# Optimization experiments

Hardware: AMD Instinct MI355X
Metric: run time of the kernel (lower is better)

The kernel has to match this reference:

```python
import jax, jax.numpy as jnp
import numpy as np

CP_SPACING = (4, 4, 4)
SIGMAS = tuple(0.44 * cp for cp in CP_SPACING)


def _gaussian_kernel_3d(sigmas):
    # Faithful to DeepReg layer_util.gaussian_filter_3d
    ks = [int(np.ceil(s * 3) + np.mod(np.ceil(s * 3) + 1, 2)) for s in sigmas]
    grid = np.stack(np.meshgrid(*[np.arange(k) for k in ks], indexing="ij"), axis=0)  # [3,k,k,k]
    mean = ((np.asarray(ks, np.float64) - 1.0) / 2.0).reshape(-1, 1, 1, 1)
    var = (np.asarray(sigmas, np.float64) ** 2.0).reshape(-1, 1, 1, 1)
    norm = 1.0 / (np.sqrt(2.0 * np.pi) ** 3 + np.prod(sigmas))  # as in DeepReg source
    kernel = norm * np.exp(-np.sum((grid - mean) ** 2.0 / (2.0 * var), axis=0))
    kernel = kernel / np.sum(kernel)  # sums to 1
    return kernel.astype(np.float32)  # [k,k,k]


def setup_inputs() -> dict:
    key = jax.random.key(0)
    image = jax.random.normal(key, (4, 160, 160, 160, 3), dtype=jnp.float32)  # DDF volume, 3 channels
    kernel = jnp.asarray(_gaussian_kernel_3d(SIGMAS))  # deterministic [7,7,7] Gaussian buffer
    return {"image": image, "kernel": kernel}


def reference(image, kernel):
    b, d1, d2, d3, c = image.shape
    # DeepReg's [k,k,k,3,3] diagonal kernel == depthwise blur per channel.
    kdw = jnp.tile(kernel[..., None, None], (1, 1, 1, 1, c))  # [k,k,k,1,C]
    blurred = jax.lax.conv_general_dilated(
        image, kdw,
        window_strides=(1, 1, 1),
        padding="SAME",
        dimension_numbers=("NDHWC", "DHWIO", "NDHWC"),
        feature_group_count=c,
    )
    # output control-point grid: ceil(dim / cp_spacing) + 3
    size = tuple(int(np.ceil(v / cp)) + 3 for v, cp in zip((d1, d2, d3), CP_SPACING))
    # tf.image.resize bilinear (TF2) uses half-pixel centers == jax.image.resize 'linear'
    out = jax.image.resize(blurred, (b,) + size + (c,), method="linear")
    return out
```

## Files before the change

kernel.cpp:

```cpp
#include <hip/hip_runtime.h>
#include <hip/hip_fp16.h>

#define NB 4
#define NI 160
#define NO 43
#define NC 3
#define KS 7
#define KPAD 3
#define MT 16
#define CH 8
#define CH1 2
#define P1B 64
#define NP 22

#define ROWF (NI * NC)
#define PROW 132
#define PROW4 (PROW / 4)
#define LROW 484
#define SLICE (NO * NO * NC)

#define A1H_BYTES ((size_t)NB * NI * NI * PROW * 2)
#define A2H_BYTES ((size_t)NB * NI * NO * PROW * 2)
#define P2P_THREADS ((size_t)NB * NI * NP * PROW4)
#define P3_THREADS ((size_t)NB * NO * NO * PROW4)

struct __align__(16) Tables {
    float w1[NO][MT];
    float wp[NP][24][2];
    int   o1hp[NP][24];
    int   o0h[NO][MT];
    int   j3[NO];
    int   jlo[NO];
};

constexpr double ctaylor(double r) {
    double s = 1.0, term = 1.0;
    for (int n = 1; n <= 13; ++n) { term *= r / (double)n; s += term; }
    return s;
}
constexpr double cexp_neg(double x) {
    double y = -x;
    int k = (int)(y * 16.0);
    double r = y - (double)k / 16.0;
    double e16 = ctaylor(1.0 / 16.0);
    double p = 1.0;
    for (int i = 0; i < k; ++i) p *= e16;
    return 1.0 / (p * ctaylor(r));
}
constexpr int cceil(double x)  { int c = (int)x; return ((double)c < x) ? c + 1 : c; }
constexpr int cfloor(double x) { int f = (int)x; return ((double)f > x) ? f - 1 : f; }
constexpr double cabsd(double x) { return x < 0 ? -x : x; }

constexpr double comp_w(int j, double sf, int ilo, int ihi, const double* g) {
    if (j >= NI || j < 0) return 0.0;
    double cw = 0.0;
    for (int t = 0; t < KS; ++t) {
        int i = j + KPAD - t;
        if (i >= ilo && i <= ihi) {
            double w = 1.0 - cabsd(sf - (double)i) * (43.0 / 160.0);
            if (w > 0.0) cw += g[t] * w;
        }
    }
    return cw;
}

struct Band { double sf; int ilo; int ihi; double wsum; };
constexpr Band bandof(int o) {
    const double inv_scale = 160.0 / 43.0;
    double sf = ((double)o + 0.5) * inv_scale - 0.5;
    int ilo = cceil(sf - inv_scale);  if (ilo < 0) ilo = 0;
    int ihi = cfloor(sf + inv_scale); if (ihi > NI - 1) ihi = NI - 1;
    double wsum = 0.0;
    for (int i = ilo; i <= ihi; ++i) {
        double w = 1.0 - cabsd(sf - (double)i) * (43.0 / 160.0);
        if (w > 0.0) wsum += w;
    }
    return {sf, ilo, ihi, wsum};
}

constexpr Tables make_tables() {
    Tables T{};
    double g[KS] = {};
    double gs = 0.0;
    const double sig = 0.44 * 4.0;
    for (int i = 0; i < KS; ++i) {
        double d = (double)i - 3.0;
        g[i] = cexp_neg(-(d * d) / (2.0 * sig * sig));
        gs += g[i];
    }
    for (int i = 0; i < KS; ++i) g[i] /= gs;

    for (int o = 0; o < NO; ++o) {
        Band B = bandof(o);
        int jlo = B.ilo - KPAD; if (jlo < 0) jlo = 0;
        T.j3[o] = jlo & ~3;
        T.jlo[o] = jlo;
        for (int k = 0; k < MT; ++k) {
            int j = jlo + k;
            T.w1[o][k] = (float)(comp_w(j, B.sf, B.ilo, B.ihi, g) / B.wsum);
            int jc = (j < NI) ? j : (NI - 1);
            T.o0h[o][k] = jc * (NO * PROW * 2);
        }
    }
    for (int p = 0; p < NP; ++p) {
        int oA = 2 * p, oB = 2 * p + 1;
        Band BA = bandof(oA);
        int jp = T.j3[oA];
        for (int k = 0; k < 24; ++k) {
            T.wp[p][k][0] = (float)(comp_w(jp + k, BA.sf, BA.ilo, BA.ihi, g) / BA.wsum);
            if (oB < NO) {
                Band BB = bandof(oB);
                T.wp[p][k][1] = (float)(comp_w(jp + k, BB.sf, BB.ilo, BB.ihi, g) / BB.wsum);
            } else {
                T.wp[p][k][1] = 0.0f;
            }
            int jc = (jp + k < NI) ? (jp + k) : (NI - 1);
            T.o1hp[p][k] = jc * (PROW * 2);
        }
    }
    return T;
}

__constant__ Tables dT = make_tables();

struct __align__(8) h4 { __half2 lo, hi; };
union h2u { __half2 h; unsigned int u; };

__global__ __launch_bounds__(P1B) void k_p1(
        const float* __restrict__ img, __half* __restrict__ A1h) {
    __shared__ __align__(16) float rows[CH1 * LROW + 64];
    int t = threadIdx.x;
    int blk = blockIdx.x;

    const int p = t % NP, row = t / NP;
    const bool has = (t < NP * CH1);

    float4 wq0, wq1, wq2, wq3, wq4, wq5, wq6, wq7, wq8, wq9, wq10, wq11;
    int jp = 0;
    if (has) {
        jp = dT.j3[2 * p];
        const float4* wpp = (const float4*)dT.wp[p];
        wq0 = wpp[0];  wq1 = wpp[1];  wq2 = wpp[2];  wq3 = wpp[3];
        wq4 = wpp[4];  wq5 = wpp[5];  wq6 = wpp[6];  wq7 = wpp[7];
        wq8 = wpp[8];  wq9 = wpp[9];  wq10 = wpp[10]; wq11 = wpp[11];
    }

    const float4* src = (const float4*)(img + (size_t)blk * (CH1 * ROWF));
    for (int g = t; g < CH1 * ROWF / 4; g += P1B) {
        int r = g / 120, m = g % 120;
        *(float4*)(rows + r * LROW + 4 * m) = src[g];
    }
    if (t < CH1 * 4) rows[(t >> 2) * LROW + ROWF + (t & 3)] = 0.f;
    rows[CH1 * LROW + t] = 0.f;
    __syncthreads();

    if (has) {
        const float4* dp = (const float4*)(rows + row * LROW + 3 * jp);
        float a0 = 0.f, a1 = 0.f, a2 = 0.f;
        float b0 = 0.f, b1 = 0.f, b2 = 0.f;
#define STEP(M, WQA, WQB) {                                                    \
            float4 v0 = dp[3*(M)], v1 = dp[3*(M)+1], v2 = dp[3*(M)+2];         \
            a0 += WQA.x * v0.x; a1 += WQA.x * v0.y; a2 += WQA.x * v0.z;        \
            b0 += WQA.y * v0.x; b1 += WQA.y * v0.y; b2 += WQA.y * v0.z;        \
            a0 += WQA.z * v0.w; a1 += WQA.z * v1.x; a2 += WQA.z * v1.y;        \
            b0 += WQA.w * v0.w; b1 += WQA.w * v1.x; b2 += WQA.w * v1.y;        \
            a0 += WQB.x * v1.z; a1 += WQB.x * v1.w; a2 += WQB.x * v2.x;        \
            b0 += WQB.y * v1.z; b1 += WQB.y * v1.w; b2 += WQB.y * v2.x;        \
            a0 += WQB.z * v2.y; a1 += WQB.z * v2.z; a2 += WQB.z * v2.w;        \
            b0 += WQB.w * v2.y; b1 += WQB.w * v2.z; b2 += WQB.w * v2.w;        \
        }
        STEP(0, wq0, wq1)  STEP(1, wq2, wq3)  STEP(2, wq4, wq5)
        STEP(3, wq6, wq7)  STEP(4, wq8, wq9)  STEP(5, wq10, wq11)
#undef STEP
        h2u c0, c1, c2;
        c0.h = __floats2half2_rn(a0, a1);
        c1.h = __floats2half2_rn(a2, b0);
        c2.h = __floats2half2_rn(b1, b2);
        unsigned int* dstu = (unsigned int*)A1h;
        size_t baseu = ((size_t)blk * CH1 + row) * (PROW / 2) + 3 * p;
        dstu[baseu] = c0.u; dstu[baseu + 1] = c1.u; dstu[baseu + 2] = c2.u;
    }
}

__device__ __forceinline__ int xcd_swz(int wg, int nwg) {
    int q = nwg >> 3, r = nwg & 7;
    int x = wg & 7, i = wg >> 3;
    return (x < r ? x * (q + 1) : r * (q + 1) + (x - r) * q) + i;
}

__global__ __launch_bounds__(256) void k_p2(
        const __half* __restrict__ A1h, __half* __restrict__ A2h) {
    int blk = xcd_swz(blockIdx.x, gridDim.x);
    size_t idx = (size_t)blk * 256 + threadIdx.x;
    if (idx >= P2P_THREADS) return;
    int ii = (int)idx;
    int col4 = ii % PROW4;
    int p    = (ii / PROW4) % NP;
    int slab = ii / (PROW4 * NP);
    const char* base = (const char*)A1h + ((size_t)slab * NI * PROW + col4 * 4) * 2;
    const float4* wpp = (const float4*)dT.wp[p];
    const int4*   ot  = (const int4*)dT.o1hp[p];
    float4 wq0 = wpp[0], wq1 = wpp[1], wq2 = wpp[2],  wq3 = wpp[3];
    float4 wq4 = wpp[4], wq5 = wpp[5], wq6 = wpp[6],  wq7 = wpp[7];
    float4 wq8 = wpp[8], wq9 = wpp[9], wq10 = wpp[10], wq11 = wpp[11];
    int4 t0 = ot[0], t1 = ot[1], t2 = ot[2], t3 = ot[3], t4 = ot[4], t5 = ot[5];
    float4 a = {0.f,0.f,0.f,0.f}, b = a;
#define TP(J, WA, WB) { h4 v = *(const h4*)(base + (unsigned)(J));             \
        float2 f0 = __half22float2(v.lo), f1 = __half22float2(v.hi);           \
        a.x += (WA) * f0.x; a.y += (WA) * f0.y;                                \
        a.z += (WA) * f1.x; a.w += (WA) * f1.y;                                \
        b.x += (WB) * f0.x; b.y += (WB) * f0.y;                                \
        b.z += (WB) * f1.x; b.w += (WB) * f1.y; }
    TP(t0.x, wq0.x, wq0.y)  TP(t0.y, wq0.z, wq0.w)
    TP(t0.z, wq1.x, wq1.y)  TP(t0.w, wq1.z, wq1.w)
    TP(t1.x, wq2.x, wq2.y)  TP(t1.y, wq2.z, wq2.w)
    TP(t1.z, wq3.x, wq3.y)  TP(t1.w, wq3.z, wq3.w)
    TP(t2.x, wq4.x, wq4.y)  TP(t2.y, wq4.z, wq4.w)
    TP(t2.z, wq5.x, wq5.y)  TP(t2.w, wq5.z, wq5.w)
    TP(t3.x, wq6.x, wq6.y)  TP(t3.y, wq6.z, wq6.w)
    TP(t3.z, wq7.x, wq7.y)  TP(t3.w, wq7.z, wq7.w)
    TP(t4.x, wq8.x, wq8.y)  TP(t4.y, wq8.z, wq8.w)
    TP(t4.z, wq9.x, wq9.y)  TP(t4.w, wq9.z, wq9.w)
    TP(t5.x, wq10.x, wq10.y) TP(t5.y, wq10.z, wq10.w)
    TP(t5.z, wq11.x, wq11.y) TP(t5.w, wq11.z, wq11.w)
#undef TP
    h4* A2h4 = (h4*)A2h;
    size_t rbase = ((size_t)slab * NO + 2 * p) * PROW4 + col4;
    h4 ra; ra.lo = __floats2half2_rn(a.x, a.y); ra.hi = __floats2half2_rn(a.z, a.w);
    A2h4[rbase] = ra;
    if (2 * p + 1 < NO) {
        h4 rb; rb.lo = __floats2half2_rn(b.x, b.y); rb.hi = __floats2half2_rn(b.z, b.w);
        A2h4[rbase + PROW4] = rb;
    }
}

__global__ __launch_bounds__(256) void k_p3(
        const __half* __restrict__ A2h, float* __restrict__ out) {
    int blk = xcd_swz(blockIdx.x, gridDim.x);
    size_t idx = (size_t)blk * 256 + threadIdx.x;
    if (idx >= P3_THREADS) return;
    int ii = (int)idx;
    int col4 = ii % PROW4;
    int o2   = (ii / PROW4) % NO;
    int o1   = (ii / (PROW4 * NO)) % NO;
    int b    = ii / (PROW4 * NO * NO);
    const char* base = (const char*)A2h +
        (((size_t)b * NI * NO + o2) * PROW + col4 * 4) * 2;
    const float4* wv = (const float4*)dT.w1[o1];
    const int4*   ov = (const int4*)dT.o0h[o1];
    float4 w0 = wv[0], w1v = wv[1], w2 = wv[2], w3 = wv[3];
    int4   j0 = ov[0], j1 = ov[1], j2 = ov[2], j3 = ov[3];
    float4 a = {0.f, 0.f, 0.f, 0.f};
#define TAP4H(J, W) { h4 v = *(const h4*)(base + (unsigned)(J));               \
                      float2 f0 = __half22float2(v.lo);                        \
                      float2 f1 = __half22float2(v.hi);                        \
                      a.x += (W) * f0.x; a.y += (W) * f0.y;                    \
                      a.z += (W) * f1.x; a.w += (W) * f1.y; }
    TAP4H(j0.x, w0.x) TAP4H(j0.y, w0.y) TAP4H(j0.z, w0.z) TAP4H(j0.w, w0.w)
    TAP4H(j1.x, w1v.x) TAP4H(j1.y, w1v.y) TAP4H(j1.z, w1v.z) TAP4H(j1.w, w1v.w)
    TAP4H(j2.x, w2.x) TAP4H(j2.y, w2.y) TAP4H(j2.z, w2.z) TAP4H(j2.w, w2.w)
    TAP4H(j3.x, w3.x) TAP4H(j3.y, w3.y) TAP4H(j3.z, w3.z) TAP4H(j3.w, w3.w)
#undef TAP4H
    int tile = (b * NO + o1) * NO + o2;
    float* ob = out + (size_t)tile * (NO * NC) + col4 * 4;
    int col = col4 * 4;
    float av[4] = {a.x, a.y, a.z, a.w};
    #pragma unroll
    for (int e = 0; e < 4; ++e)
        if (col + e < NO * NC) ob[e] = av[e];
}

__global__ __launch_bounds__(256) void k_passA(
        const float* __restrict__ img, float* __restrict__ S) {
    __shared__ float rows[CH * NI * NC];
    __shared__ float T[CH * NO * NC];
    __shared__ float acc[NO * NO * NC];
    __shared__ float w2[NO * MT];
    __shared__ int   s2[NO];
    int t = threadIdx.x;
    int blk = blockIdx.x;
    const float* src = img + (size_t)blk * (NI * NI * NC);
    for (int k = t; k < NO * MT; k += 256) w2[k] = ((const float*)dT.w1)[k];
    for (int k = t; k < NO; k += 256) s2[k] = dT.jlo[k];
    for (int k = t; k < NO * NO * NC; k += 256) acc[k] = 0.f;
    __syncthreads();
    for (int chunk = 0; chunk < NI / CH; ++chunk) {
        const float4* csrc = (const float4*)(src + (size_t)chunk * CH * NI * NC);
        for (int k = t; k < CH * NI * NC / 4; k += 256)
            ((float4*)rows)[k] = csrc[k];
        __syncthreads();
        for (int task = t; task < CH * NO; task += 256) {
            int ch = task / NO, o3 = task % NO;
            int st = s2[o3];
            const float* rp = rows + ch * NI * NC;
            float a0 = 0.f, a1 = 0.f, a2 = 0.f;
            #pragma unroll
            for (int k = 0; k < MT; ++k) {
                int j = st + k; j = (j < NI) ? j : (NI - 1);
                float w = w2[o3 * MT + k];
                a0 += w * rp[j * 3 + 0];
                a1 += w * rp[j * 3 + 1];
                a2 += w * rp[j * 3 + 2];
            }
            T[task * NC + 0] = a0;
            T[task * NC + 1] = a1;
            T[task * NC + 2] = a2;
        }
        __syncthreads();
        int i2base = chunk * CH;
        for (int task = t; task < NO * NO; task += 256) {
            int o2 = task / NO, o3 = task % NO;
            int st = s2[o2];
            int k0 = i2base - st;        k0 = (k0 > 0) ? k0 : 0;
            int k1 = i2base + CH - st;   k1 = (k1 < MT) ? k1 : MT;
            if (k1 > k0) {
                float a0 = 0.f, a1 = 0.f, a2 = 0.f;
                for (int k = k0; k < k1; ++k) {
                    float w = w2[o2 * MT + k];
                    int ch = st + k - i2base;
                    a0 += w * T[(ch * NO + o3) * NC + 0];
                    a1 += w * T[(ch * NO + o3) * NC + 1];
                    a2 += w * T[(ch * NO + o3) * NC + 2];
                }
                acc[task * NC + 0] += a0;
                acc[task * NC + 1] += a1;
                acc[task * NC + 2] += a2;
            }
        }
        __syncthreads();
    }
    float* Sp = S + (size_t)blk * (NO * NO * NC);
    for (int k = t; k < NO * NO * NC; k += 256) Sp[k] = acc[k];
}

__global__ __launch_bounds__(256) void k_passB(
        const float* __restrict__ S, float* __restrict__ out) {
    int blk = blockIdx.x;
    int b = blk / NO, o1 = blk % NO;
    __shared__ float w1s[MT];
    __shared__ int s1v;
    if (threadIdx.x < MT) w1s[threadIdx.x] = dT.w1[o1][threadIdx.x];
    if (threadIdx.x == 0) s1v = dT.jlo[o1];
    __syncthreads();
    const float* Sb = S + (size_t)b * NI * (NO * NO * NC);
    float* ob = out + (size_t)blk * (NO * NO * NC);
    int st = s1v;
    for (int e = threadIdx.x; e < NO * NO * NC; e += 256) {
        float a = 0.f;
        #pragma unroll
        for (int k = 0; k < MT; ++k) {
            int i1 = st + k; i1 = (i1 < NI) ? i1 : (NI - 1);
            a += w1s[k] * Sb[(size_t)i1 * (NO * NO * NC) + e];
        }
        ob[e] = a;
    }
}

extern "C" void kernel_launch(void* const* d_in, const int* in_sizes, int n_in,
                              void* d_out, int out_size, void* d_ws, size_t ws_size,
                              hipStream_t stream) {
    (void)in_sizes; (void)n_in; (void)out_size;
    const float* img = (const float*)d_in[0];
    float* out = (float*)d_out;
    char* ws = (char*)d_ws;

    if (ws_size >= A1H_BYTES + A2H_BYTES) {
        __half* A1h = (__half*)ws;
        __half* A2h = (__half*)(ws + A1H_BYTES);
        k_p1<<<NB * NI * (NI / CH1), P1B, 0, stream>>>(img, A1h);
        int p2b = (int)((P2P_THREADS + 255) / 256);
        k_p2<<<p2b, 256, 0, stream>>>(A1h, A2h);
        int p3b = (int)((P3_THREADS + 255) / 256);
        k_p3<<<p3b, 256, 0, stream>>>(A2h, out);
    } else {
        float* S = (float*)ws;
        k_passA<<<NB * NI, 256, 0, stream>>>(img, S);
        k_passB<<<NB * NO, 256, 0, stream>>>(S, out);
    }
}
```

Measured before the change: 65.27 us.

## Compute three output columns per thread in first pass with padded layout

The first (innermost-axis) resample pass now has each thread produce three neighbouring output control points instead of two, using a new 28-tap weight table, and processes four rows per block instead of two. The intermediate half-precision row layout changes to groups of ten halves (nine values plus one pad), widening rows from 132 to 152 halves, and the final pass remaps packed columns back to the dense output. This cuts the number of overlapping input reads per output in pass one, at the cost of more registers and about 15% more intermediate data for passes two and three.

```diff
diff --git a/kernel.cpp b/kernel.cpp
--- a/kernel.cpp
+++ b/kernel.cpp
@@ -9,27 +9,29 @@
 #define KPAD 3
 #define MT 16
 #define CH 8
-#define CH1 2
+#define CH1 4
 #define P1B 64
 #define NP 22
+#define NT 15
 
 #define ROWF (NI * NC)
-#define PROW 132
-#define PROW4 (PROW / 4)
+#define PR 152
+#define PR4 (PR / 4)
 #define LROW 484
-#define SLICE (NO * NO * NC)
-
-#define A1H_BYTES ((size_t)NB * NI * NI * PROW * 2)
-#define A2H_BYTES ((size_t)NB * NI * NO * PROW * 2)
-#define P2P_THREADS ((size_t)NB * NI * NP * PROW4)
-#define P3_THREADS ((size_t)NB * NO * NO * PROW4)
+
+#define A1H_BYTES ((size_t)NB * NI * NI * PR * 2)
+#define A2H_BYTES ((size_t)NB * NI * NO * PR * 2)
+#define P2P_THREADS ((size_t)NB * NI * NP * PR4)
+#define P3_THREADS ((size_t)NB * NO * NO * PR4)
 
 struct __align__(16) Tables {
     float w1[NO][MT];
     float wp[NP][24][2];
+    float wt[NT][84];
     int   o1hp[NP][24];
     int   o0h[NO][MT];
     int   j3[NO];
+    int   j3t[NT];
     int   jlo[NO];
 };
 
@@ -99,7 +101,7 @@
             int j = jlo + k;
             T.w1[o][k] = (float)(comp_w(j, B.sf, B.ilo, B.ihi, g) / B.wsum);
             int jc = (j < NI) ? j : (NI - 1);
-            T.o0h[o][k] = jc * (NO * PROW * 2);
+            T.o0h[o][k] = jc * (NO * PR * 2);
         }
     }
     for (int p = 0; p < NP; ++p) {
@@ -115,7 +117,23 @@
                 T.wp[p][k][1] = 0.0f;
             }
             int jc = (jp + k < NI) ? (jp + k) : (NI - 1);
-            T.o1hp[p][k] = jc * (PROW * 2);
+            T.o1hp[p][k] = jc * (PR * 2);
+        }
+    }
+    for (int q = 0; q < NT; ++q) {
+        int jq = T.jlo[3 * q] & ~3;
+        T.j3t[q] = jq;
+        for (int k = 0; k < 28; ++k) {
+            for (int m = 0; m < 3; ++m) {
+                int o = 3 * q + m;
+                if (o < NO) {
+                    Band B = bandof(o);
+                    T.wt[q][k * 3 + m] =
+                        (float)(comp_w(jq + k, B.sf, B.ilo, B.ihi, g) / B.wsum);
+                } else {
+                    T.wt[q][k * 3 + m] = 0.0f;
+                }
+            }
         }
     }
     return T;
@@ -132,17 +150,18 @@
     int t = threadIdx.x;
     int blk = blockIdx.x;
 
-    const int p = t % NP, row = t / NP;
-    const bool has = (t < NP * CH1);
-
-    float4 wq0, wq1, wq2, wq3, wq4, wq5, wq6, wq7, wq8, wq9, wq10, wq11;
+    const int q = t % NT, row = t / NT;
+    const bool has = (t < NT * CH1);
+
+    float4 w0,w1,w2,w3,w4,w5,w6,w7,w8,w9,w10,w11,w12,w13,w14,w15,w16,w17,w18,w19,w20;
     int jp = 0;
     if (has) {
-        jp = dT.j3[2 * p];
-        const float4* wpp = (const float4*)dT.wp[p];
-        wq0 = wpp[0];  wq1 = wpp[1];  wq2 = wpp[2];  wq3 = wpp[3];
-        wq4 = wpp[4];  wq5 = wpp[5];  wq6 = wpp[6];  wq7 = wpp[7];
-        wq8 = wpp[8];  wq9 = wpp[9];  wq10 = wpp[10]; wq11 = wpp[11];
+        jp = dT.j3t[q];
+        const float4* wf = (const float4*)dT.wt[q];
+        w0=wf[0];  w1=wf[1];  w2=wf[2];  w3=wf[3];  w4=wf[4];  w5=wf[5];
+        w6=wf[6];  w7=wf[7];  w8=wf[8];  w9=wf[9];  w10=wf[10]; w11=wf[11];
+        w12=wf[12]; w13=wf[13]; w14=wf[14]; w15=wf[15]; w16=wf[16]; w17=wf[17];
+        w18=wf[18]; w19=wf[19]; w20=wf[20];
     }
 
     const float4* src = (const float4*)(img + (size_t)blk * (CH1 * ROWF));
@@ -156,29 +175,37 @@
 
     if (has) {
         const float4* dp = (const float4*)(rows + row * LROW + 3 * jp);
-        float a0 = 0.f, a1 = 0.f, a2 = 0.f;
-        float b0 = 0.f, b1 = 0.f, b2 = 0.f;
-#define STEP(M, WQA, WQB) {                                                    \
-            float4 v0 = dp[3*(M)], v1 = dp[3*(M)+1], v2 = dp[3*(M)+2];         \
-            a0 += WQA.x * v0.x; a1 += WQA.x * v0.y; a2 += WQA.x * v0.z;        \
-            b0 += WQA.y * v0.x; b1 += WQA.y * v0.y; b2 += WQA.y * v0.z;        \
-            a0 += WQA.z * v0.w; a1 += WQA.z * v1.x; a2 += WQA.z * v1.y;        \
-            b0 += WQA.w * v0.w; b1 += WQA.w * v1.x; b2 += WQA.w * v1.y;        \
-            a0 += WQB.x * v1.z; a1 += WQB.x * v1.w; a2 += WQB.x * v2.x;        \
-            b0 += WQB.y * v1.z; b1 += WQB.y * v1.w; b2 += WQB.y * v2.x;        \
-            a0 += WQB.z * v2.y; a1 += WQB.z * v2.z; a2 += WQB.z * v2.w;        \
-            b0 += WQB.w * v2.y; b1 += WQB.w * v2.z; b2 += WQB.w * v2.w;        \
-        }
-        STEP(0, wq0, wq1)  STEP(1, wq2, wq3)  STEP(2, wq4, wq5)
-        STEP(3, wq6, wq7)  STEP(4, wq8, wq9)  STEP(5, wq10, wq11)
+        float a00=0.f,a01=0.f,a02=0.f, a10=0.f,a11=0.f,a12=0.f,
+              a20=0.f,a21=0.f,a22=0.f;
+#define TAP9(WM0,WM1,WM2, VC0,VC1,VC2)                                         \
+        a00 += (WM0)*(VC0); a01 += (WM0)*(VC1); a02 += (WM0)*(VC2);            \
+        a10 += (WM1)*(VC0); a11 += (WM1)*(VC1); a12 += (WM1)*(VC2);            \
+        a20 += (WM2)*(VC0); a21 += (WM2)*(VC1); a22 += (WM2)*(VC2);
+#define STEP(M, WA, WB, WC) {                                                  \
+        float4 v0 = dp[3*(M)], v1 = dp[3*(M)+1], v2 = dp[3*(M)+2];             \
+        TAP9(WA.x, WA.y, WA.z, v0.x, v0.y, v0.z)                               \
+        TAP9(WA.w, WB.x, WB.y, v0.w, v1.x, v1.y)                               \
+        TAP9(WB.z, WB.w, WC.x, v1.z, v1.w, v2.x)                               \
+        TAP9(WC.y, WC.z, WC.w, v2.y, v2.z, v2.w) }
+        STEP(0, w0,  w1,  w2)   STEP(1, w3,  w4,  w5)
+        STEP(2, w6,  w7,  w8)   STEP(3, w9,  w10, w11)
+        STEP(4, w12, w13, w14)  STEP(5, w15, w16, w17)
+        STEP(6, w18, w19, w20)
 #undef STEP
-        h2u c0, c1, c2;
-        c0.h = __floats2half2_rn(a0, a1);
-        c1.h = __floats2half2_rn(a2, b0);
-        c2.h = __floats2half2_rn(b1, b2);
+#undef TAP9
+        h2u c0, c1, c2, c3, c4;
+        c0.h = __floats2half2_rn(a00, a01);
+        c1.h = __floats2half2_rn(a02, a10);
+        c2.h = __floats2half2_rn(a11, a12);
+        c3.h = __floats2half2_rn(a20, a21);
+        c4.h = __floats2half2_rn(a22, 0.f);
         unsigned int* dstu = (unsigned int*)A1h;
-        size_t baseu = ((size_t)blk * CH1 + row) * (PROW / 2) + 3 * p;
-        dstu[baseu] = c0.u; dstu[baseu + 1] = c1.u; dstu[baseu + 2] = c2.u;
+        size_t baseu = ((size_t)blk * CH1 + row) * (PR / 2) + 5 * q;
+        dstu[baseu]     = c0.u; dstu[baseu + 1] = c1.u; dstu[baseu + 2] = c2.u;
+        dstu[baseu + 3] = c3.u; dstu[baseu + 4] = c4.u;
+    } else {
+        int r = t - NT * CH1;
+        ((unsigned int*)A1h)[((size_t)blk * CH1 + r) * (PR / 2) + 75] = 0u;
     }
 }
 
@@ -194,10 +221,10 @@
     size_t idx = (size_t)blk * 256 + threadIdx.x;
     if (idx >= P2P_THREADS) return;
     int ii = (int)idx;
-    int col4 = ii % PROW4;
-    int p    = (ii / PROW4) % NP;
-    int slab = ii / (PROW4 * NP);
-    const char* base = (const char*)A1h + ((size_t)slab * NI * PROW + col4 * 4) * 2;
+    int col4 = ii % PR4;
+    int p    = (ii / PR4) % NP;
+    int slab = ii / (PR4 * NP);
+    const char* base = (const char*)A1h + ((size_t)slab * NI * PR + col4 * 4) * 2;
     const float4* wpp = (const float4*)dT.wp[p];
     const int4*   ot  = (const int4*)dT.o1hp[p];
     float4 wq0 = wpp[0], wq1 = wpp[1], wq2 = wpp[2],  wq3 = wpp[3];
@@ -225,12 +252,12 @@
     TP(t5.z, wq11.x, wq11.y) TP(t5.w, wq11.z, wq11.w)
 #undef TP
     h4* A2h4 = (h4*)A2h;
-    size_t rbase = ((size_t)slab * NO + 2 * p) * PROW4 + col4;
+    size_t rbase = ((size_t)slab * NO + 2 * p) * PR4 + col4;
     h4 ra; ra.lo = __floats2half2_rn(a.x, a.y); ra.hi = __floats2half2_rn(a.z, a.w);
     A2h4[rbase] = ra;
     if (2 * p + 1 < NO) {
         h4 rb; rb.lo = __floats2half2_rn(b.x, b.y); rb.hi = __floats2half2_rn(b.z, b.w);
-        A2h4[rbase + PROW4] = rb;
+        A2h4[rbase + PR4] = rb;
     }
 }
 
@@ -240,12 +267,12 @@
     size_t idx = (size_t)blk * 256 + threadIdx.x;
     if (idx >= P3_THREADS) return;
     int ii = (int)idx;
-    int col4 = ii % PROW4;
-    int o2   = (ii / PROW4) % NO;
-    int o1   = (ii / (PROW4 * NO)) % NO;
-    int b    = ii / (PROW4 * NO * NO);
+    int col4 = ii % PR4;
+    int o2   = (ii / PR4) % NO;
+    int o1   = (ii / (PR4 * NO)) % NO;
+    int b    = ii / (PR4 * NO * NO);
     const char* base = (const char*)A2h +
-        (((size_t)b * NI * NO + o2) * PROW + col4 * 4) * 2;
+        (((size_t)b * NI * NO + o2) * PR + col4 * 4) * 2;
     const float4* wv = (const float4*)dT.w1[o1];
     const int4*   ov = (const int4*)dT.o0h[o1];
     float4 w0 = wv[0], w1v = wv[1], w2 = wv[2], w3 = wv[3];
@@ -262,12 +289,17 @@
     TAP4H(j3.x, w3.x) TAP4H(j3.y, w3.y) TAP4H(j3.z, w3.z) TAP4H(j3.w, w3.w)
 #undef TAP4H
     int tile = (b * NO + o1) * NO + o2;
-    float* ob = out + (size_t)tile * (NO * NC) + col4 * 4;
-    int col = col4 * 4;
+    float* ob = out + (size_t)tile * (NO * NC);
     float av[4] = {a.x, a.y, a.z, a.w};
     #pragma unroll
-    for (int e = 0; e < 4; ++e)
-        if (col + e < NO * NC) ob[e] = av[e];
+    for (int e = 0; e < 4; ++e) {
+        int pc = col4 * 4 + e;
+        int g = pc / 10, r = pc % 10;
+        if (r < 9) {
+            int oc = g * 9 + r;
+            if (oc < NO * NC) ob[oc] = av[e];
+        }
+    }
 }
 
 __global__ __launch_bounds__(256) void k_passA(
```

Result: slower. 80.11 us (+22.7%).
